# Performance work log

Measured on AMD Instinct MI355X. Metric: run time of the kernel, lower is better.

## Reference

```python
import jax, jax.numpy as jnp
import numpy as np

# Mamba2(d_model=256, headdim=32) defaults: d_state=128, d_conv=4, expand=2, ngroups=1, chunk=256
B, CIN, L = 8, 256, 1024
D_MODEL = CIN
D_INNER = 2 * D_MODEL            # expand=2 -> 512
HEADDIM = 32
NHEADS = D_INNER // HEADDIM      # 16
D_STATE = 128
D_CONV = 4
CONV_DIM = D_INNER + 2 * D_STATE             # 768 (ngroups=1)
D_IN_PROJ = 2 * D_INNER + 2 * D_STATE + NHEADS  # 1296
GN_GROUPS = 8
CHUNK = 256
EPS = 1e-5

def setup_inputs():
    key = jax.random.key(0)
    ks = jax.random.split(key, 8)
    x = jax.random.normal(ks[0], (B, CIN, L), jnp.float32)
    W_in = jax.random.normal(ks[1], (D_IN_PROJ, D_MODEL), jnp.float32) * 0.02
    conv_w = jax.random.normal(ks[2], (CONV_DIM, D_CONV), jnp.float32) * 0.2
    conv_b = jax.random.normal(ks[3], (CONV_DIM,), jnp.float32) * 0.02
    dt = jnp.exp(jax.random.uniform(ks[4], (NHEADS,)) * (jnp.log(0.1) - jnp.log(0.001)) + jnp.log(0.001))
    dt_bias = dt + jnp.log(-jnp.expm1(-dt))   # inverse softplus
    A_log = jnp.log(jax.random.uniform(ks[5], (NHEADS,), minval=1.0, maxval=16.0))
    Dp = jnp.ones((NHEADS,), jnp.float32)
    rms_w = jnp.ones((D_INNER,), jnp.float32)
    W_out = jax.random.normal(ks[6], (D_MODEL, D_INNER), jnp.float32) * 0.02
    gn_w = jnp.ones((CIN,), jnp.float32)
    gn_b = jnp.zeros((CIN,), jnp.float32)
    return dict(x=x, W_in=W_in, conv_w=conv_w, conv_b=conv_b, dt_bias=dt_bias,
                A_log=A_log, Dp=Dp, rms_w=rms_w, W_out=W_out, gn_w=gn_w, gn_b=gn_b)

def segsum(a):
    # a: (..., T) -> (..., T, T) with sum_{j<i<=t} a_i on/below diagonal, -inf above
    T = a.shape[-1]
    cs = jnp.cumsum(a, -1)
    d = cs[..., :, None] - cs[..., None, :]
    mask = jnp.tril(jnp.ones((T, T), bool))
    return jnp.where(mask, d, -jnp.inf)

def ssd(X, A, Bm, Cm):
    # X: (b,l,h,p) already dt-scaled; A: (b,l,h) = dt*A_cont; Bm,Cm: (b,l,n) (ngroups=1)
    b, l, h, p = X.shape
    n = Bm.shape[-1]
    c = l // CHUNK
    X = X.reshape(b, c, CHUNK, h, p)
    A = A.reshape(b, c, CHUNK, h).transpose(0, 3, 1, 2)      # (b,h,c,l)
    Bm = Bm.reshape(b, c, CHUNK, n)
    Cm = Cm.reshape(b, c, CHUNK, n)
    A_cs = jnp.cumsum(A, -1)                                  # (b,h,c,l)
    Lmat = jnp.exp(segsum(A))                                 # (b,h,c,l,l)
    Y_diag = jnp.einsum('bcln,bcsn,bhcls,bcshp->bclhp', Cm, Bm, Lmat, X)
    decay_states = jnp.exp(A_cs[..., -1:] - A_cs)             # (b,h,c,l)
    states = jnp.einsum('bcln,bhcl,bclhp->bchpn', Bm, decay_states, X)
    decay_chunk = jnp.exp(segsum(jnp.pad(A_cs[..., -1], ((0, 0), (0, 0), (1, 0)))))  # (b,h,c+1,c+1)
    states = jnp.concatenate([jnp.zeros_like(states[:, :1]), states], axis=1)        # (b,c+1,h,p,n)
    prev = jnp.einsum('bhzc,bchpn->bzhpn', decay_chunk, states)[:, :-1]              # (b,c,h,p,n)
    Y_off = jnp.einsum('bcln,bchpn,bhcl->bclhp', Cm, prev, jnp.exp(A_cs))
    return (Y_diag + Y_off).reshape(b, l, h, p)

def _forward(x, W_in, conv_w, conv_b, dt_bias, A_log, Dp, rms_w, W_out, gn_w, gn_b):
    u = jnp.transpose(x, (0, 2, 1))                           # (B,L,d_model)
    zxbcdt = u @ W_in.T                                       # (B,L,1296)
    z = zxbcdt[..., :D_INNER]
    xBC = zxbcdt[..., D_INNER:D_INNER + CONV_DIM]
    dt = jax.nn.softplus(zxbcdt[..., D_INNER + CONV_DIM:] + dt_bias)  # (B,L,H)
    # causal depthwise conv1d + SiLU
    xpad = jnp.pad(xBC, ((0, 0), (D_CONV - 1, 0), (0, 0)))
    xconv = conv_b + sum(conv_w[:, k] * xpad[:, k:k + L, :] for k in range(D_CONV))
    xconv = jax.nn.silu(xconv)
    xs = xconv[..., :D_INNER].reshape(B, L, NHEADS, HEADDIM)
    Bm = xconv[..., D_INNER:D_INNER + D_STATE]
    Cm = xconv[..., D_INNER + D_STATE:]
    A = -jnp.exp(A_log)                                       # (H,)
    Y = ssd(dt[..., None] * xs, dt * A, Bm, Cm)               # (B,L,H,P)
    Y = Y + xs * Dp[None, None, :, None]
    # gated RMSNorm (norm_before_gate=False): rmsnorm(y * silu(z)) * weight
    y = Y.reshape(B, L, D_INNER) * jax.nn.silu(z)
    y = y * jax.lax.rsqrt(jnp.mean(y * y, -1, keepdims=True) + EPS) * rms_w
    out = jnp.transpose(y @ W_out.T, (0, 2, 1))               # (B,C,L)
    # GroupNorm(8, C) over (channels_per_group, L)
    og = out.reshape(B, GN_GROUPS, CIN // GN_GROUPS, L)
    mu = og.mean((2, 3), keepdims=True)
    var = og.var((2, 3), keepdims=True)
    out = ((og - mu) * jax.lax.rsqrt(var + EPS)).reshape(B, CIN, L)
    out = out * gn_w[None, :, None] + gn_b[None, :, None]
    return out * jnp.tanh(jax.nn.softplus(out))               # Mish

def reference(x, W_in, conv_w, conv_b, dt_bias, A_log, Dp, rms_w, W_out, gn_w, gn_b):
    return _forward(x, W_in, conv_w, conv_b, dt_bias, A_log, Dp, rms_w, W_out, gn_w, gn_b)
```

## Files before the change

### kernel.cpp

```cpp
#include <hip/hip_runtime.h>
#include <hip/hip_bf16.h>
#include <math.h>

#define B_ 8
#define L_ 1024
#define DM 256
#define DI 512
#define HD 32
#define NH 16
#define DS 128
#define CDIM 768
#define NZX 1280
#define CH 256
#define NC 4
#define M_ (B_*L_)
#define EPSV 1e-5f

typedef short bf16x8 __attribute__((ext_vector_type(8)));
typedef float f32x4 __attribute__((ext_vector_type(4)));

#define OFF_ZX   0
#define SZ_ZX    (M_*NZX/2)
#define OFF_XC   (OFF_ZX+SZ_ZX)
#define SZ_XC    (M_*CDIM/2)
#define OFF_DT   (OFF_XC+SZ_XC)
#define SZ_DT    (M_*NH)
#define OFF_ACS  (OFF_DT+SZ_DT)
#define SZ_ACS   (B_*NC*NH*CH)
#define OFF_S0   (OFF_ACS+SZ_ACS)
#define SZ_S0    (B_*NC*CH*CH/2)
#define OFF_ST   (OFF_S0+SZ_S0)
#define SZ_ST    (B_*NC*NH*HD*DS)
#define OFF_PV   (OFF_ST+SZ_ST)
#define SZ_PV    SZ_ST
#define OFF_Y    (OFF_PV+SZ_PV)
#define SZ_Y     (M_*DI/2)
#define OFF_YNB  (OFF_Y+SZ_Y)
#define SZ_YNB   (M_*DI/2)
#define OFF_XBF  (OFF_YNB+SZ_YNB)
#define SZ_XBF   (M_*DM/2)
#define OFF_WBF  (OFF_XBF+SZ_XBF)
#define SZ_WBF   (1296*DM/2)
#define OFF_WOBF (OFF_WBF+SZ_WBF)
#define SZ_WOBF  (DM*DI/2)
#define OFF_GNP  (OFF_WOBF+SZ_WOBF)
#define SZ_GNP   (64*2)
#define OFF_BT   (OFF_GNP+SZ_GNP)
#define SZ_BT    (32*128*256/2)
#define OFF_OUTB (OFF_BT+SZ_BT)
#define SZ_OUTB  (M_*DM/2)

__device__ __forceinline__ ushort f2bf(float v) {
  __hip_bfloat16 h = __float2bfloat16(v);
  return *(ushort*)&h;
}
__device__ __forceinline__ float bf2f(ushort u) {
  return __uint_as_float(((unsigned int)u) << 16);
}

__global__ __launch_bounds__(256) void k_prep(const float* __restrict__ x,
                                              const float* __restrict__ W_in,
                                              const float* __restrict__ W_out,
                                              ushort* __restrict__ xbf,
                                              ushort* __restrict__ wbf,
                                              ushort* __restrict__ wobf,
                                              float2* __restrict__ gnp) {
  __shared__ float Ts[64][65];
  const int bid = blockIdx.x;
  const int t = threadIdx.x;
  if (bid < 512) {
    const int kt = bid & 3, lt = (bid >> 2) & 15, b = bid >> 6;
    const int k0 = kt*64, l0 = lt*64;
    for (int i = t; i < 4096; i += 256) {
      int kk = i>>6, ll = i&63;
      Ts[kk][ll] = x[(size_t)b*DM*L_ + (size_t)(k0+kk)*L_ + l0+ll];
    }
    __syncthreads();
    for (int i = t; i < 4096; i += 256) {
      int mm = i>>6, kk = i&63;
      xbf[(size_t)(b*L_ + l0+mm)*DM + k0+kk] = f2bf(Ts[kk][mm]);
    }
  } else if (bid < 512 + 1296) {
    int i = (bid-512)*256 + t;
    if (i < 1296*DM) wbf[i] = f2bf(W_in[i]);
  } else if (bid < 512 + 1296 + 512) {
    int i = (bid-512-1296)*256 + t;
    wobf[i] = f2bf(W_out[i]);
  } else {
    if (t < 64) gnp[t] = make_float2(0.f, 0.f);
  }
}

__global__ __launch_bounds__(256) void k_gemm_in_mfma(const ushort* __restrict__ xbf,
                                                      const ushort* __restrict__ wbf,
                                                      ushort* __restrict__ zxb) {
  __shared__ ushort As[128*40];
  __shared__ ushort Bs[64*40];
  const int tid = threadIdx.x;
  const int n0 = blockIdx.x*64, m0 = blockIdx.y*128;
  const int wave = tid>>6, lane = tid&63;
  const int lr = lane&15, quad = lane>>4;
  const int KK = DM;
  f32x4 acc[2][4];
#pragma unroll
  for (int mi=0;mi<2;++mi)
#pragma unroll
    for (int ni=0;ni<4;++ni)
#pragma unroll
      for (int r=0;r<4;++r) acc[mi][ni][r] = 0.f;
  const int srow = tid>>2, sc = tid&3;
  for (int k0 = 0; k0 < KK; k0 += 32) {
    *(uint4*)&As[srow*40 + sc*8]      = *(const uint4*)(xbf + (size_t)(m0+srow)*KK    + k0 + sc*8);
    *(uint4*)&As[(srow+64)*40 + sc*8] = *(const uint4*)(xbf + (size_t)(m0+srow+64)*KK + k0 + sc*8);
    *(uint4*)&Bs[srow*40 + sc*8]      = *(const uint4*)(wbf + (size_t)(n0+srow)*KK    + k0 + sc*8);
    __syncthreads();
    bf16x8 af[2], bfr[4];
    const int ar = wave*32 + lr;
    af[0] = *(const bf16x8*)&As[ar*40 + quad*8];
    af[1] = *(const bf16x8*)&As[(ar+16)*40 + quad*8];
#pragma unroll
    for (int ni=0;ni<4;++ni) bfr[ni] = *(const bf16x8*)&Bs[(ni*16+lr)*40 + quad*8];
#pragma unroll
    for (int mi=0;mi<2;++mi)
#pragma unroll
      for (int ni=0;ni<4;++ni)
        acc[mi][ni] = __builtin_amdgcn_mfma_f32_16x16x32_bf16(af[mi], bfr[ni], acc[mi][ni], 0, 0, 0);
    __syncthreads();
  }
#pragma unroll
  for (int mi=0;mi<2;++mi) {
    int m = m0 + wave*32 + mi*16 + quad*4;
#pragma unroll
    for (int ni=0;ni<4;++ni) {
      int n = n0 + ni*16 + lr;
#pragma unroll
      for (int r=0;r<4;++r) zxb[(size_t)(m+r)*NZX + n] = f2bf(acc[mi][ni][r]);
    }
  }
}

__global__ __launch_bounds__(256) void k_dt_direct(const float* __restrict__ x,
                                                   const float* __restrict__ W,
                                                   const float* __restrict__ dt_bias,
                                                   float* __restrict__ dtb) {
  __shared__ float Xs[256][16];
  __shared__ float Ws[16][257];
  const int t = threadIdx.x;
  const int bm = blockIdx.x*16;
  const int b = bm >> 10, l0 = bm & 1023;
  for (int i = t; i < 4096; i += 256) {
    int h = i>>8, k = i&255;
    Ws[h][k] = W[(size_t)(NZX+h)*DM + k];
  }
  for (int i = t; i < 4096; i += 256) {
    int k = i>>4, li = i&15;
    Xs[k][li] = x[(size_t)b*DM*L_ + (size_t)k*L_ + l0+li];
  }
  __syncthreads();
  const int h = t&15, li = t>>4;
  float acc = 0.f;
#pragma unroll 8
  for (int k = 0; k < 256; ++k) acc += Xs[k][li]*Ws[h][k];
  float v = acc + dt_bias[h];
  dtb[(size_t)bm*NH + t] = (v > 20.f) ? v : log1pf(expf(v));
}

__global__ __launch_bounds__(256) void k_conv(const ushort* __restrict__ zxb,
                                              const float* __restrict__ cw,
                                              const float* __restrict__ cb,
                                              ushort* __restrict__ xcb,
                                              ushort* __restrict__ btg) {
  const int j = blockIdx.x*256 + threadIdx.x;
  const int m8 = blockIdx.y*8;
  const int l0 = m8 & 1023;
  const int mb = m8 & ~1023;
  const float4 w = *(const float4*)&cw[j*4];
  const float bias = cb[j];
  float v[11];
#pragma unroll
  for (int i = 0; i < 11; ++i) {
    int ll = l0 - 3 + i;
    v[i] = (ll >= 0) ? bf2f(zxb[(size_t)(mb+ll)*NZX + DI + j]) : 0.f;
  }
  union { ushort u[8]; uint4 q; } res;
#pragma unroll
  for (int i = 0; i < 8; ++i) {
    float a = bias + w.x*v[i] + w.y*v[i+1] + w.z*v[i+2] + w.w*v[i+3];
    a = a / (1.f + expf(-a));
    res.u[i] = f2bf(a);
    xcb[(size_t)(mb+l0+i)*CDIM + j] = res.u[i];
  }
  if (j >= DI && j < DI+DS) {
    const int n = j - DI;
    const int bc = (mb >> 10)*NC + (l0 >> 8);
    const int lc = l0 & 255;
    *(uint4*)&btg[((size_t)bc*DS + n)*CH + lc] = res.q;
  }
}

__global__ __launch_bounds__(256) void k_s0_mfma(const ushort* __restrict__ xcb,
                                                 ushort* __restrict__ S0b) {
  const int lt = blockIdx.x, st = blockIdx.y, bc = blockIdx.z;
  if (st > lt) return;
  const int base = bc*CH;
  const int t = threadIdx.x;
  const int wave = t>>6, lane = t&63, lr = lane&15, quad = lane>>4;
  const int l = lt*64 + wave*16 + lr;
  f32x4 acc[4];
#pragma unroll
  for (int nt = 0; nt < 4; ++nt)
#pragma unroll
    for (int r = 0; r < 4; ++r) acc[nt][r] = 0.f;
#pragma unroll
  for (int ks = 0; ks < 4; ++ks) {
    bf16x8 af = *(const bf16x8*)(xcb + (size_t)(base+l)*CDIM + (DI+DS) + ks*32 + quad*8);
#pragma unroll
    for (int nt = 0; nt < 4; ++nt) {
      bf16x8 bf = *(const bf16x8*)(xcb + (size_t)(base + st*64 + nt*16 + lr)*CDIM + DI + ks*32 + quad*8);
      acc[nt] = __builtin_amdgcn_mfma_f32_16x16x32_bf16(af, bf, acc[nt], 0, 0, 0);
    }
  }
#pragma unroll
  for (int nt = 0; nt < 4; ++nt)
#pragma unroll
    for (int r = 0; r < 4; ++r)
      S0b[((size_t)bc*CH + lt*64 + wave*16 + quad*4 + r)*CH + st*64 + nt*16 + lr] = f2bf(acc[nt][r]);
}

__global__ __launch_bounds__(256) void k_states_mfma(const ushort* __restrict__ xcb,
                                                     const ushort* __restrict__ btg,
                                                     const float* __restrict__ dtb,
                                                     const float* __restrict__ A_log,
                                                     float* __restrict__ acs_g,
                                                     float* __restrict__ st) {
  __shared__ float acs[CH];
  __shared__ ushort Xw[32][264];
  const int t = threadIdx.x;
  const int bc = blockIdx.x, h = blockIdx.y;
  const int base = bc*CH;
  float dt_t = dtb[(size_t)(base+t)*NH + h];
  float An = -expf(A_log[h]);
  acs[t] = dt_t * An;
  __syncthreads();
  for (int off = 1; off < CH; off <<= 1) {
    float v = (t >= off) ? acs[t-off] : 0.f;
    __syncthreads();
    acs[t] += v;
    __syncthreads();
  }
  float alast = acs[CH-1];
  acs_g[((size_t)bc*NH + h)*CH + t] = acs[t];
  float w = expf(alast - acs[t]) * dt_t;
  {
    const ushort* xp = xcb + (size_t)(base+t)*CDIM + h*HD;
    ushort tmp[32];
    *(uint4*)&tmp[0]  = *(const uint4*)(xp);
    *(uint4*)&tmp[8]  = *(const uint4*)(xp+8);
    *(uint4*)&tmp[16] = *(const uint4*)(xp+16);
    *(uint4*)&tmp[24] = *(const uint4*)(xp+24);
#pragma unroll
    for (int p = 0; p < 32; ++p) Xw[p][t] = f2bf(bf2f(tmp[p]) * w);
  }
  __syncthreads();
  const int wave = t>>6, lane = t&63, lr = lane&15, quad = lane>>4;
  f32x4 acc[2][2];
#pragma unroll
  for (int mt=0;mt<2;++mt)
#pragma unroll
    for (int nt=0;nt<2;++nt)
#pragma unroll
      for (int r=0;r<4;++r) acc[mt][nt][r] = 0.f;
  const ushort* bp = btg + (size_t)bc*DS*CH;
#pragma unroll
  for (int k0 = 0; k0 < CH; k0 += 32) {
    bf16x8 a0 = *(const bf16x8*)&Xw[lr][k0 + quad*8];
    bf16x8 a1 = *(const bf16x8*)&Xw[16+lr][k0 + quad*8];
    bf16x8 b0 = *(const bf16x8*)(bp + (size_t)(wave*32 + lr)*CH + k0 + quad*8);
    bf16x8 b1 = *(const bf16x8*)(bp + (size_t)(wave*32 + 16 + lr)*CH + k0 + quad*8);
    acc[0][0] = __builtin_amdgcn_mfma_f32_16x16x32_bf16(a0, b0, acc[0][0], 0,0,0);
    acc[0][1] = __builtin_amdgcn_mfma_f32_16x16x32_bf16(a0, b1, acc[0][1], 0,0,0);
    acc[1][0] = __builtin_amdgcn_mfma_f32_16x16x32_bf16(a1, b0, acc[1][0], 0,0,0);
    acc[1][1] = __builtin_amdgcn_mfma_f32_16x16x32_bf16(a1, b1, acc[1][1], 0,0,0);
  }
  size_t sb = ((size_t)bc*NH + h)*HD*DS;
#pragma unroll
  for (int mt = 0; mt < 2; ++mt)
#pragma unroll
    for (int nt = 0; nt < 2; ++nt)
#pragma unroll
      for (int r = 0; r < 4; ++r)
        st[sb + (size_t)(mt*16 + quad*4 + r)*DS + wave*32 + nt*16 + lr] = acc[mt][nt][r];
}

__global__ void k_scan(const float* __restrict__ acs_g, const float* __restrict__ st,
                       float* __restrict__ pv) {
  const int b = blockIdx.x, h = blockIdx.y;
  const int t = threadIdx.x;
  float P[16];
#pragma unroll
  for (int i = 0; i < 16; ++i) P[i] = 0.f;
  for (int c = 0; c < NC; ++c) {
    size_t sb = ((size_t)(b*NC+c)*NH + h)*HD*DS;
    float T = acs_g[((size_t)(b*NC+c)*NH + h)*CH + (CH-1)];
    float ec = expf(T);
#pragma unroll
    for (int i = 0; i < 16; ++i) {
      size_t e = sb + (size_t)i*256 + t;
      pv[e] = P[i];
      P[i] = st[e] + ec * P[i];
    }
  }
}

__global__ __launch_bounds__(256) void k_y_mfma(const ushort* __restrict__ xcb,
    const float* __restrict__ dtb, const float* __restrict__ acs_g,
    const ushort* __restrict__ S0b, const float* __restrict__ pv,
    const float* __restrict__ Dp, ushort* __restrict__ Yb) {
  __shared__ ushort Xt[32][280];
  __shared__ float acs[CH];
  __shared__ float dts[CH];
  __shared__ float E8[CH];
  const int t = threadIdx.x;
  const int bc = blockIdx.x, h = blockIdx.y;
  const int base = bc*CH;
  acs[t] = acs_g[((size_t)bc*NH + h)*CH + t];
  dts[t] = dtb[(size_t)(base+t)*NH + h];
  {
    const ushort* xp = xcb + (size_t)(base+t)*CDIM + h*HD;
    ushort tmp[32];
    *(uint4*)&tmp[0]  = *(const uint4*)(xp);
    *(uint4*)&tmp[8]  = *(const uint4*)(xp+8);
    *(uint4*)&tmp[16] = *(const uint4*)(xp+16);
    *(uint4*)&tmp[24] = *(const uint4*)(xp+24);
#pragma unroll
    for (int p = 0; p < 32; ++p) Xt[p][t] = tmp[p];
  }
  __syncthreads();
  E8[t] = expf(acs[t & ~7] - acs[t]) * dts[t];
  __syncthreads();
  const int wave = t>>6, lane = t&63, lr = lane&15, quad = lane>>4;
  f32x4 acc[4][2];
#pragma unroll
  for (int mt=0;mt<4;++mt)
#pragma unroll
    for (int nt=0;nt<2;++nt)
#pragma unroll
      for (int r=0;r<4;++r) acc[mt][nt][r] = 0.f;
  const size_t pb = ((size_t)bc*NH + h)*HD*DS;
#pragma unroll
  for (int ks = 0; ks < 4; ++ks) {
    bf16x8 bfr[2];
#pragma unroll
    for (int nt = 0; nt < 2; ++nt) {
      const float* pp = pv + pb + (size_t)(nt*16+lr)*DS + ks*32 + quad*8;
      float4 v0 = *(const float4*)pp;
      float4 v1 = *(const float4*)(pp+4);
      bf16x8 bb;
      bb[0]=(short)f2bf(v0.x); bb[1]=(short)f2bf(v0.y); bb[2]=(short)f2bf(v0.z); bb[3]=(short)f2bf(v0.w);
      bb[4]=(short)f2bf(v1.x); bb[5]=(short)f2bf(v1.y); bb[6]=(short)f2bf(v1.z); bb[7]=(short)f2bf(v1.w);
      bfr[nt] = bb;
    }
#pragma unroll
    for (int mt = 0; mt < 4; ++mt) {
      int l = wave*64 + mt*16 + lr;
      bf16x8 af = *(const bf16x8*)(xcb + (size_t)(base+l)*CDIM + (DI+DS) + ks*32 + quad*8);
      acc[mt][0] = __builtin_amdgcn_mfma_f32_16x16x32_bf16(af, bfr[0], acc[mt][0], 0,0,0);
      acc[mt][1] = __builtin_amdgcn_mfma_f32_16x16x32_bf16(af, bfr[1], acc[mt][1], 0,0,0);
    }
  }
#pragma unroll
  for (int mt = 0; mt < 4; ++mt)
#pragma unroll
    for (int r = 0; r < 4; ++r) {
      float e = expf(acs[wave*64 + mt*16 + quad*4 + r]);
      acc[mt][0][r] *= e;
      acc[mt][1][r] *= e;
    }
  float al[4];
#pragma unroll
  for (int mt = 0; mt < 4; ++mt) al[mt] = acs[wave*64 + mt*16 + lr];
  const int km3 = 2*wave + 1;
  for (int ks = 0; ks <= km3; ++ks) {
    const int sq = ks*32 + quad*8;
    const float as0 = acs[sq];
    const float4 e0 = *(const float4*)&E8[sq];
    const float4 e1 = *(const float4*)&E8[sq+4];
    const bf16x8 xb0 = *(const bf16x8*)&Xt[lr][sq];
    const bf16x8 xb1 = *(const bf16x8*)&Xt[16+lr][sq];
    const float ev[8] = {e0.x,e0.y,e0.z,e0.w,e1.x,e1.y,e1.z,e1.w};
#pragma unroll
    for (int mt = 0; mt < 4; ++mt) {
      if (ks > ((wave*64 + mt*16 + 15) >> 5)) continue;
      const int l = wave*64 + mt*16 + lr;
      const bf16x8 sb = *(const bf16x8*)(S0b + ((size_t)bc*CH + l)*CH + sq);
      const float el = expf(al[mt] - as0);
      bf16x8 mf;
#pragma unroll
      for (int j = 0; j < 8; ++j) {
        float v = (sq + j <= l) ? bf2f((ushort)sb[j]) * el * ev[j] : 0.f;
        mf[j] = (short)f2bf(v);
      }
      acc[mt][0] = __builtin_amdgcn_mfma_f32_16x16x32_bf16(mf, xb0, acc[mt][0], 0,0,0);
      acc[mt][1] = __builtin_amdgcn_mfma_f32_16x16x32_bf16(mf, xb1, acc[mt][1], 0,0,0);
    }
  }
  const float dph = Dp[h];
#pragma unroll
  for (int mt = 0; mt < 4; ++mt) {
    const int lb = wave*64 + mt*16 + quad*4;
#pragma unroll
    for (int nt = 0; nt < 2; ++nt) {
      const int p = nt*16 + lr;
#pragma unroll
      for (int r = 0; r < 4; ++r) {
        float xv = bf2f(Xt[p][lb+r]);
        Yb[(size_t)(base+lb+r)*DI + h*HD + p] = f2bf(acc[mt][nt][r] + dph*xv);
      }
    }
  }
}

__global__ __launch_bounds__(256) void k_rms(const ushort* __restrict__ zxb,
                                             const ushort* __restrict__ Yb,
                                             const float* __restrict__ rw,
                                             ushort* __restrict__ yn) {
  const int m = blockIdx.x, t = threadIdx.x;
  float z0 = bf2f(zxb[(size_t)m*NZX + t]);
  float z1 = bf2f(zxb[(size_t)m*NZX + t + 256]);
  float y0 = bf2f(Yb[(size_t)m*DI + t])       * z0 / (1.f + expf(-z0));
  float y1 = bf2f(Yb[(size_t)m*DI + t + 256]) * z1 / (1.f + expf(-z1));
  float ss = y0*y0 + y1*y1;
#pragma unroll
  for (int off = 32; off > 0; off >>= 1) ss += __shfl_down(ss, off);
  __shared__ float red[4];
  __shared__ float sinv;
  if ((t & 63) == 0) red[t >> 6] = ss;
  __syncthreads();
  if (t == 0) sinv = rsqrtf((red[0]+red[1]+red[2]+red[3]) * (1.f/DI) + EPSV);
  __syncthreads();
  float inv = sinv;
  yn[(size_t)m*DI + t]       = f2bf(y0 * inv * rw[t]);
  yn[(size_t)m*DI + t + 256] = f2bf(y1 * inv * rw[t+256]);
}

__global__ __launch_bounds__(256) void k_gemm_out_mfma(const ushort* __restrict__ ynbf,
                                                       const ushort* __restrict__ wobf,
                                                       ushort* __restrict__ outb,
                                                       float2* __restrict__ gnp) {
  __shared__ ushort As[128*40];
  __shared__ ushort Bs[64*40];
  const int tid = threadIdx.x;
  const int n0 = blockIdx.x*64, m0 = blockIdx.y*128;
  const int wave = tid>>6, lane = tid&63;
  const int lr = lane&15, quad = lane>>4;
  const int KK = DI;
  f32x4 acc[2][4];
#pragma unroll
  for (int mi=0;mi<2;++mi)
#pragma unroll
    for (int ni=0;ni<4;++ni)
#pragma unroll
      for (int r=0;r<4;++r) acc[mi][ni][r] = 0.f;
  const int srow = tid>>2, sc = tid&3;
  for (int k0 = 0; k0 < KK; k0 += 32) {
    *(uint4*)&As[srow*40 + sc*8]      = *(const uint4*)(ynbf + (size_t)(m0+srow)*KK    + k0 + sc*8);
    *(uint4*)&As[(srow+64)*40 + sc*8] = *(const uint4*)(ynbf + (size_t)(m0+srow+64)*KK + k0 + sc*8);
    *(uint4*)&Bs[srow*40 + sc*8]      = *(const uint4*)(wobf + (size_t)(n0+srow)*KK    + k0 + sc*8);
    __syncthreads();
    bf16x8 af[2], bfr[4];
    const int ar = wave*32 + lr;
    af[0] = *(const bf16x8*)&As[ar*40 + quad*8];
    af[1] = *(const bf16x8*)&As[(ar+16)*40 + quad*8];
#pragma unroll
    for (int ni=0;ni<4;++ni) bfr[ni] = *(const bf16x8*)&Bs[(ni*16+lr)*40 + quad*8];
#pragma unroll
    for (int mi=0;mi<2;++mi)
#pragma unroll
      for (int ni=0;ni<4;++ni)
        acc[mi][ni] = __builtin_amdgcn_mfma_f32_16x16x32_bf16(af[mi], bfr[ni], acc[mi][ni], 0, 0, 0);
    __syncthreads();
  }
  const int b = m0 >> 10, l0 = m0 & 1023;
  float s0=0.f, ss0=0.f, s1=0.f, ss1=0.f;
#pragma unroll
  for (int mi=0;mi<2;++mi) {
    int lb = l0 + wave*32 + mi*16 + quad*4;
#pragma unroll
    for (int ni=0;ni<4;++ni) {
      int n = n0 + ni*16 + lr;
      union { ushort u[4]; uint2 q; } pk;
#pragma unroll
      for (int r=0;r<4;++r) pk.u[r] = f2bf(acc[mi][ni][r]);
      *(uint2*)&outb[(size_t)b*DM*L_ + (size_t)n*L_ + lb] = pk.q;
      float ps = acc[mi][ni][0]+acc[mi][ni][1]+acc[mi][ni][2]+acc[mi][ni][3];
      float pq = acc[mi][ni][0]*acc[mi][ni][0]+acc[mi][ni][1]*acc[mi][ni][1]
               + acc[mi][ni][2]*acc[mi][ni][2]+acc[mi][ni][3]*acc[mi][ni][3];
      if (ni < 2) { s0 += ps; ss0 += pq; } else { s1 += ps; ss1 += pq; }
    }
  }
#pragma unroll
  for (int off = 32; off > 0; off >>= 1) {
    s0 += __shfl_down(s0, off); ss0 += __shfl_down(ss0, off);
    s1 += __shfl_down(s1, off); ss1 += __shfl_down(ss1, off);
  }
  __shared__ float red[4][4];
  if (lane == 0) { red[wave][0]=s0; red[wave][1]=ss0; red[wave][2]=s1; red[wave][3]=ss1; }
  __syncthreads();
  if (tid == 0) {
    float S0=0,Q0=0,S1=0,Q1=0;
#pragma unroll
    for (int wv2 = 0; wv2 < 4; ++wv2) { S0+=red[wv2][0]; Q0+=red[wv2][1]; S1+=red[wv2][2]; Q1+=red[wv2][3]; }
    int g0 = b*8 + (n0>>5);
    atomicAdd(&gnp[g0].x, S0);   atomicAdd(&gnp[g0].y, Q0);
    atomicAdd(&gnp[g0+1].x, S1); atomicAdd(&gnp[g0+1].y, Q1);
  }
}

__global__ __launch_bounds__(256) void k_gn_apply(const float2* __restrict__ gnp,
                                                  const float* __restrict__ gw,
                                                  const float* __restrict__ gb,
                                                  const ushort* __restrict__ ob,
                                                  float* __restrict__ o) {
  const int ch = blockIdx.x & 255, b = blockIdx.x >> 8;
  const int t = threadIdx.x;
  float2 p = gnp[b*8 + (ch>>5)];
  const float mean = p.x * (1.f/(32.f*L_));
  const float var  = p.y * (1.f/(32.f*L_)) - mean*mean;
  const float inv  = rsqrtf(var + EPSV);
  const float w = gw[ch], bb = gb[ch];
  size_t base = (size_t)blockIdx.x * L_;
  ushort4 v = *(const ushort4*)&ob[base + t*4];
  float r[4] = {bf2f(v.x), bf2f(v.y), bf2f(v.z), bf2f(v.w)};
#pragma unroll
  for (int j = 0; j < 4; ++j) {
    float u = (r[j] - mean) * inv * w + bb;
    float m;
    if (u > 15.f) m = u;
    else {
      float e = expf(u);
      float a = 1.f + e;
      float a2 = a*a;
      m = u * (a2 - 1.f) / (a2 + 1.f);
    }
    r[j] = m;
  }
  *(float4*)&o[base + t*4] = make_float4(r[0], r[1], r[2], r[3]);
}

extern "C" void kernel_launch(void* const* d_in, const int* in_sizes, int n_in,
                              void* d_out, int out_size, void* d_ws, size_t ws_size,
                              hipStream_t stream) {
  const float* x       = (const float*)d_in[0];
  const float* W_in    = (const float*)d_in[1];
  const float* conv_w  = (const float*)d_in[2];
  const float* conv_b  = (const float*)d_in[3];
  const float* dt_bias = (const float*)d_in[4];
  const float* A_log   = (const float*)d_in[5];
  const float* Dp      = (const float*)d_in[6];
  const float* rms_w   = (const float*)d_in[7];
  const float* W_out   = (const float*)d_in[8];
  const float* gn_w    = (const float*)d_in[9];
  const float* gn_b    = (const float*)d_in[10];
  float* out = (float*)d_out;
  float* ws  = (float*)d_ws;

  ushort* zxb   = (ushort*)(ws + OFF_ZX);
  ushort* xcb   = (ushort*)(ws + OFF_XC);
  float*  dtb   = ws + OFF_DT;
  float*  acs   = ws + OFF_ACS;
  ushort* S0b   = (ushort*)(ws + OFF_S0);
  float*  st    = ws + OFF_ST;
  float*  pv    = ws + OFF_PV;
  ushort* Ybb   = (ushort*)(ws + OFF_Y);
  ushort* ynbf  = (ushort*)(ws + OFF_YNB);
  ushort* xbf   = (ushort*)(ws + OFF_XBF);
  ushort* wbf   = (ushort*)(ws + OFF_WBF);
  ushort* wobf  = (ushort*)(ws + OFF_WOBF);
  float2* gnp   = (float2*)(ws + OFF_GNP);
  ushort* btg   = (ushort*)(ws + OFF_BT);
  ushort* outb  = (ushort*)(ws + OFF_OUTB);

  k_prep         <<<dim3(512+1296+512+1), 256, 0, stream>>>(x, W_in, W_out, xbf, wbf, wobf, gnp);
  k_gemm_in_mfma <<<dim3(NZX/64, M_/128), 256, 0, stream>>>(xbf, wbf, zxb);
  k_dt_direct    <<<dim3(M_/16), 256, 0, stream>>>(x, W_in, dt_bias, dtb);
  k_conv         <<<dim3(3, M_/8), 256, 0, stream>>>(zxb, conv_w, conv_b, xcb, btg);
  k_s0_mfma      <<<dim3(4, 4, B_*NC), 256, 0, stream>>>(xcb, S0b);
  k_states_mfma  <<<dim3(B_*NC, NH), 256, 0, stream>>>(xcb, btg, dtb, A_log, acs, st);
  k_scan         <<<dim3(B_, NH), 256, 0, stream>>>(acs, st, pv);
  k_y_mfma       <<<dim3(B_*NC, NH), 256, 0, stream>>>(xcb, dtb, acs, S0b, pv, Dp, Ybb);
  k_rms          <<<dim3(M_), 256, 0, stream>>>(zxb, Ybb, rms_w, ynbf);
  k_gemm_out_mfma<<<dim3(DM/64, M_/128), 256, 0, stream>>>(ynbf, wobf, outb, gnp);
  k_gn_apply     <<<dim3(B_*DM), 256, 0, stream>>>(gnp, gn_w, gn_b, outb, out);
}
```

Baseline: 191.9 us.

## Fuse dt projection into prep, drop scan kernel, double-buffer GEMMs

Moves the dt projection into the prep kernel as extra blocks. Removes the inter-chunk scan kernel: chunk states are now stored in bf16 and each y block rebuilds its incoming state as a decay-weighted sum of earlier chunk states. Both GEMMs get double-buffered LDS with one barrier per k-step, and the input GEMM uses 128-wide N tiles. The changes save two launches and the fp32 state traffic, at the cost of redundant state summation, larger shared memory in k_prep, and bf16 rounding of states before they are summed.

```diff
diff --git a/kernel.cpp b/kernel.cpp
--- a/kernel.cpp
+++ b/kernel.cpp
@@ -30,10 +30,8 @@
 #define OFF_S0   (OFF_ACS+SZ_ACS)
 #define SZ_S0    (B_*NC*CH*CH/2)
 #define OFF_ST   (OFF_S0+SZ_S0)
-#define SZ_ST    (B_*NC*NH*HD*DS)
-#define OFF_PV   (OFF_ST+SZ_ST)
-#define SZ_PV    SZ_ST
-#define OFF_Y    (OFF_PV+SZ_PV)
+#define SZ_ST    (B_*NC*NH*HD*DS/2)
+#define OFF_Y    (OFF_ST+SZ_ST)
 #define SZ_Y     (M_*DI/2)
 #define OFF_YNB  (OFF_Y+SZ_Y)
 #define SZ_YNB   (M_*DI/2)
@@ -61,11 +59,15 @@
 __global__ __launch_bounds__(256) void k_prep(const float* __restrict__ x,
                                               const float* __restrict__ W_in,
                                               const float* __restrict__ W_out,
+                                              const float* __restrict__ dt_bias,
                                               ushort* __restrict__ xbf,
                                               ushort* __restrict__ wbf,
                                               ushort* __restrict__ wobf,
-                                              float2* __restrict__ gnp) {
+                                              float2* __restrict__ gnp,
+                                              float* __restrict__ dtb) {
   __shared__ float Ts[64][65];
+  __shared__ float Xs[256][16];
+  __shared__ float Ws[16][257];
   const int bid = blockIdx.x;
   const int t = threadIdx.x;
   if (bid < 512) {
@@ -86,83 +88,79 @@
   } else if (bid < 512 + 1296 + 512) {
     int i = (bid-512-1296)*256 + t;
     wobf[i] = f2bf(W_out[i]);
+  } else if (bid == 2320) {
+    if (t < 64) gnp[t] = make_float2(0.f, 0.f);
   } else {
-    if (t < 64) gnp[t] = make_float2(0.f, 0.f);
+    const int bm = (bid - 2321)*16;
+    const int b = bm >> 10, l0 = bm & 1023;
+    for (int i = t; i < 4096; i += 256) {
+      int h = i>>8, k = i&255;
+      Ws[h][k] = W_in[(size_t)(NZX+h)*DM + k];
+    }
+    for (int i = t; i < 4096; i += 256) {
+      int k = i>>4, li = i&15;
+      Xs[k][li] = x[(size_t)b*DM*L_ + (size_t)k*L_ + l0+li];
+    }
+    __syncthreads();
+    const int h = t&15, li = t>>4;
+    float acc = 0.f;
+#pragma unroll 8
+    for (int k = 0; k < 256; ++k) acc += Xs[k][li]*Ws[h][k];
+    float v = acc + dt_bias[h];
+    dtb[(size_t)bm*NH + t] = (v > 20.f) ? v : log1pf(expf(v));
   }
 }
 
 __global__ __launch_bounds__(256) void k_gemm_in_mfma(const ushort* __restrict__ xbf,
                                                       const ushort* __restrict__ wbf,
                                                       ushort* __restrict__ zxb) {
-  __shared__ ushort As[128*40];
-  __shared__ ushort Bs[64*40];
+  __shared__ ushort As[2][128*40];
+  __shared__ ushort Bs[2][128*40];
   const int tid = threadIdx.x;
-  const int n0 = blockIdx.x*64, m0 = blockIdx.y*128;
+  const int n0 = blockIdx.x*128, m0 = blockIdx.y*128;
   const int wave = tid>>6, lane = tid&63;
   const int lr = lane&15, quad = lane>>4;
-  const int KK = DM;
-  f32x4 acc[2][4];
+  f32x4 acc[2][8];
 #pragma unroll
   for (int mi=0;mi<2;++mi)
 #pragma unroll
-    for (int ni=0;ni<4;++ni)
+    for (int ni=0;ni<8;++ni)
 #pragma unroll
       for (int r=0;r<4;++r) acc[mi][ni][r] = 0.f;
-  const int srow = tid>>2, sc = tid&3;
-  for (int k0 = 0; k0 < KK; k0 += 32) {
-    *(uint4*)&As[srow*40 + sc*8]      = *(const uint4*)(xbf + (size_t)(m0+srow)*KK    + k0 + sc*8);
-    *(uint4*)&As[(srow+64)*40 + sc*8] = *(const uint4*)(xbf + (size_t)(m0+srow+64)*KK + k0 + sc*8);
-    *(uint4*)&Bs[srow*40 + sc*8]      = *(const uint4*)(wbf + (size_t)(n0+srow)*KK    + k0 + sc*8);
+  const int srow = tid>>1, sc = (tid&1)*16;
+  auto LOAD = [&](int buf, int k0) {
+    *(uint4*)&As[buf][srow*40 + sc]     = *(const uint4*)(xbf + (size_t)(m0+srow)*DM + k0 + sc);
+    *(uint4*)&As[buf][srow*40 + sc + 8] = *(const uint4*)(xbf + (size_t)(m0+srow)*DM + k0 + sc + 8);
+    *(uint4*)&Bs[buf][srow*40 + sc]     = *(const uint4*)(wbf + (size_t)(n0+srow)*DM + k0 + sc);
+    *(uint4*)&Bs[buf][srow*40 + sc + 8] = *(const uint4*)(wbf + (size_t)(n0+srow)*DM + k0 + sc + 8);
+  };
+  LOAD(0, 0);
+#pragma unroll
+  for (int i = 0; i < 8; ++i) {
     __syncthreads();
-    bf16x8 af[2], bfr[4];
-    const int ar = wave*32 + lr;
-    af[0] = *(const bf16x8*)&As[ar*40 + quad*8];
-    af[1] = *(const bf16x8*)&As[(ar+16)*40 + quad*8];
-#pragma unroll
-    for (int ni=0;ni<4;++ni) bfr[ni] = *(const bf16x8*)&Bs[(ni*16+lr)*40 + quad*8];
+    if (i < 7) LOAD((i+1)&1, (i+1)*32);
+    const int cur = i&1;
+    bf16x8 af[2], bfr[8];
+    af[0] = *(const bf16x8*)&As[cur][(wave*32+lr)*40 + quad*8];
+    af[1] = *(const bf16x8*)&As[cur][(wave*32+16+lr)*40 + quad*8];
+#pragma unroll
+    for (int ni=0;ni<8;++ni) bfr[ni] = *(const bf16x8*)&Bs[cur][(ni*16+lr)*40 + quad*8];
 #pragma unroll
     for (int mi=0;mi<2;++mi)
 #pragma unroll
-      for (int ni=0;ni<4;++ni)
+      for (int ni=0;ni<8;++ni)
         acc[mi][ni] = __builtin_amdgcn_mfma_f32_16x16x32_bf16(af[mi], bfr[ni], acc[mi][ni], 0, 0, 0);
-    __syncthreads();
   }
 #pragma unroll
   for (int mi=0;mi<2;++mi) {
     int m = m0 + wave*32 + mi*16 + quad*4;
 #pragma unroll
-    for (int ni=0;ni<4;++ni) {
+    for (int ni=0;ni<8;++ni) {
       int n = n0 + ni*16 + lr;
 #pragma unroll
       for (int r=0;r<4;++r) zxb[(size_t)(m+r)*NZX + n] = f2bf(acc[mi][ni][r]);
     }
   }
-}
-
-__global__ __launch_bounds__(256) void k_dt_direct(const float* __restrict__ x,
-                                                   const float* __restrict__ W,
-                                                   const float* __restrict__ dt_bias,
-                                                   float* __restrict__ dtb) {
-  __shared__ float Xs[256][16];
-  __shared__ float Ws[16][257];
-  const int t = threadIdx.x;
-  const int bm = blockIdx.x*16;
-  const int b = bm >> 10, l0 = bm & 1023;
-  for (int i = t; i < 4096; i += 256) {
-    int h = i>>8, k = i&255;
-    Ws[h][k] = W[(size_t)(NZX+h)*DM + k];
-  }
-  for (int i = t; i < 4096; i += 256) {
-    int k = i>>4, li = i&15;
-    Xs[k][li] = x[(size_t)b*DM*L_ + (size_t)k*L_ + l0+li];
-  }
-  __syncthreads();
-  const int h = t&15, li = t>>4;
-  float acc = 0.f;
-#pragma unroll 8
-  for (int k = 0; k < 256; ++k) acc += Xs[k][li]*Ws[h][k];
-  float v = acc + dt_bias[h];
-  dtb[(size_t)bm*NH + t] = (v > 20.f) ? v : log1pf(expf(v));
 }
 
 __global__ __launch_bounds__(256) void k_conv(const ushort* __restrict__ zxb,
@@ -232,7 +230,7 @@
                                                      const float* __restrict__ dtb,
                                                      const float* __restrict__ A_log,
                                                      float* __restrict__ acs_g,
-                                                     float* __restrict__ st) {
+                                                     ushort* __restrict__ stb) {
   __shared__ float acs[CH];
   __shared__ ushort Xw[32][264];
   const int t = threadIdx.x;
@@ -289,32 +287,12 @@
     for (int nt = 0; nt < 2; ++nt)
 #pragma unroll
       for (int r = 0; r < 4; ++r)
-        st[sb + (size_t)(mt*16 + quad*4 + r)*DS + wave*32 + nt*16 + lr] = acc[mt][nt][r];
-}
-
-__global__ void k_scan(const float* __restrict__ acs_g, const float* __restrict__ st,
-                       float* __restrict__ pv) {
-  const int b = blockIdx.x, h = blockIdx.y;
-  const int t = threadIdx.x;
-  float P[16];
-#pragma unroll
-  for (int i = 0; i < 16; ++i) P[i] = 0.f;
-  for (int c = 0; c < NC; ++c) {
-    size_t sb = ((size_t)(b*NC+c)*NH + h)*HD*DS;
-    float T = acs_g[((size_t)(b*NC+c)*NH + h)*CH + (CH-1)];
-    float ec = expf(T);
-#pragma unroll
-    for (int i = 0; i < 16; ++i) {
-      size_t e = sb + (size_t)i*256 + t;
-      pv[e] = P[i];
-      P[i] = st[e] + ec * P[i];
-    }
-  }
+        stb[sb + (size_t)(mt*16 + quad*4 + r)*DS + wave*32 + nt*16 + lr] = f2bf(acc[mt][nt][r]);
 }
 
 __global__ __launch_bounds__(256) void k_y_mfma(const ushort* __restrict__ xcb,
     const float* __restrict__ dtb, const float* __restrict__ acs_g,
-    const ushort* __restrict__ S0b, const float* __restrict__ pv,
+    const ushort* __restrict__ S0b, const ushort* __restrict__ stb,
     const float* __restrict__ Dp, ushort* __restrict__ Yb) {
   __shared__ ushort Xt[32][280];
   __shared__ float acs[CH];
@@ -323,6 +301,7 @@
   const int t = threadIdx.x;
   const int bc = blockIdx.x, h = blockIdx.y;
   const int base = bc*CH;
+  const int cc = bc & 3, bc4 = bc & ~3;
   acs[t] = acs_g[((size_t)bc*NH + h)*CH + t];
   dts[t] = dtb[(size_t)(base+t)*NH + h];
   {
@@ -346,36 +325,51 @@
     for (int nt=0;nt<2;++nt)
 #pragma unroll
       for (int r=0;r<4;++r) acc[mt][nt][r] = 0.f;
-  const size_t pb = ((size_t)bc*NH + h)*HD*DS;
-#pragma unroll
-  for (int ks = 0; ks < 4; ++ks) {
-    bf16x8 bfr[2];
-#pragma unroll
-    for (int nt = 0; nt < 2; ++nt) {
-      const float* pp = pv + pb + (size_t)(nt*16+lr)*DS + ks*32 + quad*8;
-      float4 v0 = *(const float4*)pp;
-      float4 v1 = *(const float4*)(pp+4);
-      bf16x8 bb;
-      bb[0]=(short)f2bf(v0.x); bb[1]=(short)f2bf(v0.y); bb[2]=(short)f2bf(v0.z); bb[3]=(short)f2bf(v0.w);
-      bb[4]=(short)f2bf(v1.x); bb[5]=(short)f2bf(v1.y); bb[6]=(short)f2bf(v1.z); bb[7]=(short)f2bf(v1.w);
-      bfr[nt] = bb;
-    }
-#pragma unroll
-    for (int mt = 0; mt < 4; ++mt) {
-      int l = wave*64 + mt*16 + lr;
-      bf16x8 af = *(const bf16x8*)(xcb + (size_t)(base+l)*CDIM + (DI+DS) + ks*32 + quad*8);
-      acc[mt][0] = __builtin_amdgcn_mfma_f32_16x16x32_bf16(af, bfr[0], acc[mt][0], 0,0,0);
-      acc[mt][1] = __builtin_amdgcn_mfma_f32_16x16x32_bf16(af, bfr[1], acc[mt][1], 0,0,0);
-    }
-  }
-#pragma unroll
-  for (int mt = 0; mt < 4; ++mt)
-#pragma unroll
-    for (int r = 0; r < 4; ++r) {
-      float e = expf(acs[wave*64 + mt*16 + quad*4 + r]);
-      acc[mt][0][r] *= e;
-      acc[mt][1][r] *= e;
-    }
+  if (cc > 0) {
+    float fj[3];
+    {
+      float cum = 0.f;
+      for (int j = cc-1; j >= 0; --j) {
+        fj[j] = expf(cum);
+        cum += acs_g[((size_t)(bc4+j)*NH + h)*CH + (CH-1)];
+      }
+    }
+#pragma unroll
+    for (int ks = 0; ks < 4; ++ks) {
+      bf16x8 bfr[2];
+#pragma unroll
+      for (int nt = 0; nt < 2; ++nt) {
+        float P[8];
+#pragma unroll
+        for (int jj = 0; jj < 8; ++jj) P[jj] = 0.f;
+        for (int j = 0; j < cc; ++j) {
+          bf16x8 sv = *(const bf16x8*)(stb + ((size_t)(bc4+j)*NH + h)*HD*DS
+                                       + (size_t)(nt*16+lr)*DS + ks*32 + quad*8);
+#pragma unroll
+          for (int jj = 0; jj < 8; ++jj) P[jj] += fj[j]*bf2f((ushort)sv[jj]);
+        }
+        bf16x8 bb;
+#pragma unroll
+        for (int jj = 0; jj < 8; ++jj) bb[jj] = (short)f2bf(P[jj]);
+        bfr[nt] = bb;
+      }
+#pragma unroll
+      for (int mt = 0; mt < 4; ++mt) {
+        int l = wave*64 + mt*16 + lr;
+        bf16x8 af = *(const bf16x8*)(xcb + (size_t)(base+l)*CDIM + (DI+DS) + ks*32 + quad*8);
+        acc[mt][0] = __builtin_amdgcn_mfma_f32_16x16x32_bf16(af, bfr[0], acc[mt][0], 0,0,0);
+        acc[mt][1] = __builtin_amdgcn_mfma_f32_16x16x32_bf16(af, bfr[1], acc[mt][1], 0,0,0);
+      }
+    }
+#pragma unroll
+    for (int mt = 0; mt < 4; ++mt)
+#pragma unroll
+      for (int r = 0; r < 4; ++r) {
+        float e = expf(acs[wave*64 + mt*16 + quad*4 + r]);
+        acc[mt][0][r] *= e;
+        acc[mt][1][r] *= e;
+      }
+  }
   float al[4];
 #pragma unroll
   for (int mt = 0; mt < 4; ++mt) al[mt] = acs[wave*64 + mt*16 + lr];
@@ -447,13 +441,12 @@
                                                        const ushort* __restrict__ wobf,
                                                        ushort* __restrict__ outb,
                                                        float2* __restrict__ gnp) {
-  __shared__ ushort As[128*40];
-  __shared__ ushort Bs[64*40];
+  __shared__ ushort As[2][128*40];
+  __shared__ ushort Bs[2][64*40];
   const int tid = threadIdx.x;
   const int n0 = blockIdx.x*64, m0 = blockIdx.y*128;
   const int wave = tid>>6, lane = tid&63;
   const int lr = lane&15, quad = lane>>4;
-  const int KK = DI;
   f32x4 acc[2][4];
 #pragma unroll
   for (int mi=0;mi<2;++mi)
@@ -461,24 +454,29 @@
     for (int ni=0;ni<4;++ni)
 #pragma unroll
       for (int r=0;r<4;++r) acc[mi][ni][r] = 0.f;
-  const int srow = tid>>2, sc = tid&3;
-  for (int k0 = 0; k0 < KK; k0 += 32) {
-    *(uint4*)&As[srow*40 + sc*8]      = *(const uint4*)(ynbf + (size_t)(m0+srow)*KK    + k0 + sc*8);
-    *(uint4*)&As[(srow+64)*40 + sc*8] = *(const uint4*)(ynbf + (size_t)(m0+srow+64)*KK + k0 + sc*8);
-    *(uint4*)&Bs[srow*40 + sc*8]      = *(const uint4*)(wobf + (size_t)(n0+srow)*KK    + k0 + sc*8);
+  const int srow = tid>>1, sc = (tid&1)*16;
+  const int brow = tid>>2, bcol = (tid&3)*8;
+  auto LOAD = [&](int buf, int k0) {
+    *(uint4*)&As[buf][srow*40 + sc]     = *(const uint4*)(ynbf + (size_t)(m0+srow)*DI + k0 + sc);
+    *(uint4*)&As[buf][srow*40 + sc + 8] = *(const uint4*)(ynbf + (size_t)(m0+srow)*DI + k0 + sc + 8);
+    *(uint4*)&Bs[buf][brow*40 + bcol]   = *(const uint4*)(wobf + (size_t)(n0+brow)*DI + k0 + bcol);
+  };
+  LOAD(0, 0);
+#pragma unroll
+  for (int i = 0; i < 16; ++i) {
     __syncthreads();
+    if (i < 15) LOAD((i+1)&1, (i+1)*32);
+    const int cur = i&1;
     bf16x8 af[2], bfr[4];
-    const int ar = wave*32 + lr;
-    af[0] = *(const bf16x8*)&As[ar*40 + quad*8];
-    af[1] = *(const bf16x8*)&As[(ar+16)*40 + quad*8];
-#pragma unroll
-    for (int ni=0;ni<4;++ni) bfr[ni] = *(const bf16x8*)&Bs[(ni*16+lr)*40 + quad*8];
+    af[0] = *(const bf16x8*)&As[cur][(wave*32+lr)*40 + quad*8];
+    af[1] = *(const bf16x8*)&As[cur][(wave*32+16+lr)*40 + quad*8];
+#pragma unroll
+    for (int ni=0;ni<4;++ni) bfr[ni] = *(const bf16x8*)&Bs[cur][(ni*16+lr)*40 + quad*8];
 #pragma unroll
     for (int mi=0;mi<2;++mi)
 #pragma unroll
       for (int ni=0;ni<4;++ni)
         acc[mi][ni] = __builtin_amdgcn_mfma_f32_16x16x32_bf16(af[mi], bfr[ni], acc[mi][ni], 0, 0, 0);
-    __syncthreads();
   }
   const int b = m0 >> 10, l0 = m0 & 1023;
   float s0=0.f, ss0=0.f, s1=0.f, ss1=0.f;
@@ -569,8 +567,7 @@
   float*  dtb   = ws + OFF_DT;
   float*  acs   = ws + OFF_ACS;
   ushort* S0b   = (ushort*)(ws + OFF_S0);
-  float*  st    = ws + OFF_ST;
-  float*  pv    = ws + OFF_PV;
+  ushort* stb   = (ushort*)(ws + OFF_ST);
   ushort* Ybb   = (ushort*)(ws + OFF_Y);
   ushort* ynbf  = (ushort*)(ws + OFF_YNB);
   ushort* xbf   = (ushort*)(ws + OFF_XBF);
@@ -580,14 +577,13 @@
   ushort* btg   = (ushort*)(ws + OFF_BT);
   ushort* outb  = (ushort*)(ws + OFF_OUTB);
 
-  k_prep         <<<dim3(512+1296+512+1), 256, 0, stream>>>(x, W_in, W_out, xbf, wbf, wobf, gnp);
-  k_gemm_in_mfma <<<dim3(NZX/64, M_/128), 256, 0, stream>>>(xbf, wbf, zxb);
-  k_dt_direct    <<<dim3(M_/16), 256, 0, stream>>>(x, W_in, dt_bias, dtb);
+  k_prep         <<<dim3(512+1296+512+1+512), 256, 0, stream>>>(x, W_in, W_out, dt_bias,
+                                                                xbf, wbf, wobf, gnp, dtb);
+  k_gemm_in_mfma <<<dim3(NZX/128, M_/128), 256, 0, stream>>>(xbf, wbf, zxb);
   k_conv         <<<dim3(3, M_/8), 256, 0, stream>>>(zxb, conv_w, conv_b, xcb, btg);
   k_s0_mfma      <<<dim3(4, 4, B_*NC), 256, 0, stream>>>(xcb, S0b);
-  k_states_mfma  <<<dim3(B_*NC, NH), 256, 0, stream>>>(xcb, btg, dtb, A_log, acs, st);
-  k_scan         <<<dim3(B_, NH), 256, 0, stream>>>(acs, st, pv);
-  k_y_mfma       <<<dim3(B_*NC, NH), 256, 0, stream>>>(xcb, dtb, acs, S0b, pv, Dp, Ybb);
+  k_states_mfma  <<<dim3(B_*NC, NH), 256, 0, stream>>>(xcb, btg, dtb, A_log, acs, stb);
+  k_y_mfma       <<<dim3(B_*NC, NH), 256, 0, stream>>>(xcb, dtb, acs, S0b, stb, Dp, Ybb);
   k_rms          <<<dim3(M_), 256, 0, stream>>>(zxb, Ybb, rms_w, ynbf);
   k_gemm_out_mfma<<<dim3(DM/64, M_/128), 256, 0, stream>>>(ynbf, wobf, outb, gnp);
   k_gn_apply     <<<dim3(B_*DM), 256, 0, stream>>>(gnp, gn_w, gn_b, outb, out);
```

Result: no change. 192.1 us (+0.1%).
